# Optimization experiments

Hardware: AMD Instinct MI355X
Metric: run time of the kernel (lower is better)

The kernel has to match this reference:

```python
import jax, jax.numpy as jnp
import numpy as np


def setup_inputs() -> dict:
    key = jax.random.key(0)
    k1, k2, k3, k4 = jax.random.split(key, 4)
    bs, seq_len, num_heads, head_dim, num_pages = 16, 4096, 16, 128, 32768
    q = jax.random.normal(k1, (bs, num_heads, 1, head_dim), dtype=jnp.float32)
    kv_cache = jax.random.normal(k2, (2, num_pages, num_heads, head_dim), dtype=jnp.float32)
    k_indices = jax.random.randint(k3, (bs, seq_len), 0, num_pages, dtype=jnp.int64)
    v_indices = jax.random.randint(k4, (bs, seq_len), 0, num_pages, dtype=jnp.int64)
    return {"q": q, "kv_cache": kv_cache, "k_indices": k_indices, "v_indices": v_indices}


def reference(q, kv_cache, k_indices, v_indices):
    # Gather per-token K/V rows from the paged cache.
    k_cache = kv_cache[0]                      # [P, H, D]
    v_cache = kv_cache[1]                      # [P, H, D]
    k = k_cache[k_indices]                     # [B, S, H, D]
    v = v_cache[v_indices]                     # [B, S, H, D]
    head_dim = q.shape[-1]
    scale = 1.0 / jnp.sqrt(jnp.asarray(head_dim, dtype=q.dtype))
    # scores: [B, H, Q, S] (Q == 1 for decode); SDPA default: no mask, non-causal.
    scores = jnp.einsum("bhqd,bshd->bhqs", q, k) * scale
    probs = jax.nn.softmax(scores, axis=-1)
    out = jnp.einsum("bhqs,bshd->bhqd", probs, v)  # [B, H, Q, D]
    return out
```

## Files before the change

### kernel.cpp

```cpp
#include <hip/hip_runtime.h>
#include <math.h>

#define B 16
#define S 4096
#define H 16
#define D 128
#define P 32768

#define NSPLIT 8
#define WAVES_PER_BLOCK 4
#define TOK_PER_BLOCK (S / NSPLIT)
#define TOK_PER_WAVE (TOK_PER_BLOCK / WAVES_PER_BLOCK)

__global__ __launch_bounds__(256) void pa_partial(
    const float* __restrict__ q,
    const float* __restrict__ kv,
    const int* __restrict__ kidx,
    const int* __restrict__ vidx,
    float* __restrict__ ws)
{
    const int split = blockIdx.x;
    const int h     = blockIdx.y;
    const int b     = blockIdx.z;
    const int wave  = threadIdx.x >> 6;
    const int lane  = threadIdx.x & 63;

    const float scale = 0.08838834764831845f;

    const float* kbase = kv;
    const float* vbase = kv + (size_t)P * H * D;

    const float2 qv = *reinterpret_cast<const float2*>(
        q + ((size_t)b * H + h) * D + lane * 2);

    float  m   = -INFINITY;
    float  l   = 0.f;
    float2 acc = make_float2(0.f, 0.f);

    const int s0 = split * TOK_PER_BLOCK + wave * TOK_PER_WAVE;

    for (int half = 0; half < TOK_PER_WAVE / 64; ++half) {
        const int sbase = s0 + half * 64;
        const int myk = kidx[(size_t)b * S + sbase + lane];
        const int myv = vidx[(size_t)b * S + sbase + lane];

        #pragma unroll 4
        for (int t = 0; t < 64; ++t) {
            const int kp = __shfl(myk, t);
            const int vp = __shfl(myv, t);

            const float2 kvv = *reinterpret_cast<const float2*>(
                kbase + ((size_t)kp * H + h) * D + lane * 2);
            const float2 vvv = *reinterpret_cast<const float2*>(
                vbase + ((size_t)vp * H + h) * D + lane * 2);

            float partial = qv.x * kvv.x + qv.y * kvv.y;
            #pragma unroll
            for (int off = 32; off > 0; off >>= 1)
                partial += __shfl_xor(partial, off);

            const float score = partial * scale;
            const float mnew  = fmaxf(m, score);
            const float alpha = __expf(m - mnew);
            const float p     = __expf(score - mnew);
            l     = l * alpha + p;
            acc.x = acc.x * alpha + p * vvv.x;
            acc.y = acc.y * alpha + p * vvv.y;
            m     = mnew;
        }
    }

    __shared__ float lds_m[WAVES_PER_BLOCK];
    __shared__ float lds_l[WAVES_PER_BLOCK];
    __shared__ float lds_acc[WAVES_PER_BLOCK][D];

    lds_acc[wave][lane * 2]     = acc.x;
    lds_acc[wave][lane * 2 + 1] = acc.y;
    if (lane == 0) { lds_m[wave] = m; lds_l[wave] = l; }
    __syncthreads();

    float* out = ws + ((size_t)(b * H + h) * NSPLIT + split) * (D + 2);
    if (threadIdx.x < D) {
        const int d = threadIdx.x;
        const float M = fmaxf(fmaxf(lds_m[0], lds_m[1]),
                              fmaxf(lds_m[2], lds_m[3]));
        float L = 0.f, a = 0.f;
        #pragma unroll
        for (int w = 0; w < WAVES_PER_BLOCK; ++w) {
            const float e = __expf(lds_m[w] - M);
            L += lds_l[w] * e;
            a += lds_acc[w][d] * e;
        }
        out[d] = a;
        if (d == 0) { out[D] = M; out[D + 1] = L; }
    }
}

__global__ __launch_bounds__(128) void pa_reduce(
    const float* __restrict__ ws, float* __restrict__ out)
{
    const int bh = blockIdx.x;
    const int d  = threadIdx.x;
    const float* base = ws + (size_t)bh * NSPLIT * (D + 2);

    float M = -INFINITY;
    #pragma unroll
    for (int i = 0; i < NSPLIT; ++i)
        M = fmaxf(M, base[i * (D + 2) + D]);

    float L = 0.f, a = 0.f;
    #pragma unroll
    for (int i = 0; i < NSPLIT; ++i) {
        const float e = __expf(base[i * (D + 2) + D] - M);
        L += base[i * (D + 2) + D + 1] * e;
        a += base[i * (D + 2) + d] * e;
    }
    out[(size_t)bh * D + d] = a / L;
}

extern "C" void kernel_launch(void* const* d_in, const int* in_sizes, int n_in,
                              void* d_out, int out_size, void* d_ws, size_t ws_size,
                              hipStream_t stream) {
    const float* q    = (const float*)d_in[0];
    const float* kv   = (const float*)d_in[1];
    const int*   kidx = (const int*)d_in[2];
    const int*   vidx = (const int*)d_in[3];
    float*       out  = (float*)d_out;
    float*       ws   = (float*)d_ws;

    dim3 grid1(NSPLIT, H, B);
    pa_partial<<<grid1, 256, 0, stream>>>(q, kv, kidx, vidx, ws);
    pa_reduce<<<B * H, 128, 0, stream>>>(ws, out);
}
```

Baseline: 155.4 us.

## Counting-sort tokens by page to deduplicate KV reads and split K/V passes

Replaces the fused split-K flash-decode kernel with a seven-launch pipeline. It histograms, scans and scatters token indices into page-sorted lists, so each K page is read once as a full all-heads row and shared across batches and heads. V is gathered per batch in sorted page order. A K pass writes unnormalised exp(score) without subtracting a running max, a V pass accumulates weighted partial sums, and a final kernel normalises them. The intent is to cut scattered 512-byte gather traffic and reread K pages. The cost is many extra launches, atomics, an insertion-sort fixup and workspace traffic, and dropping max subtraction risks overflow for inputs with large scores.

```diff
diff --git a/kernel.cpp b/kernel.cpp
--- a/kernel.cpp
+++ b/kernel.cpp
@@ -1,121 +1,226 @@
 #include <hip/hip_runtime.h>
-#include <math.h>
 
 #define B 16
 #define S 4096
 #define H 16
 #define D 128
 #define P 32768
-
-#define NSPLIT 8
-#define WAVES_PER_BLOCK 4
-#define TOK_PER_BLOCK (S / NSPLIT)
-#define TOK_PER_WAVE (TOK_PER_BLOCK / WAVES_PER_BLOCK)
-
-__global__ __launch_bounds__(256) void pa_partial(
-    const float* __restrict__ q,
-    const float* __restrict__ kv,
-    const int* __restrict__ kidx,
-    const int* __restrict__ vidx,
-    float* __restrict__ ws)
-{
-    const int split = blockIdx.x;
-    const int h     = blockIdx.y;
-    const int b     = blockIdx.z;
-    const int wave  = threadIdx.x >> 6;
-    const int lane  = threadIdx.x & 63;
-
-    const float scale = 0.08838834764831845f;
-
-    const float* kbase = kv;
-    const float* vbase = kv + (size_t)P * H * D;
-
-    const float2 qv = *reinterpret_cast<const float2*>(
-        q + ((size_t)b * H + h) * D + lane * 2);
-
-    float  m   = -INFINITY;
-    float  l   = 0.f;
-    float2 acc = make_float2(0.f, 0.f);
-
-    const int s0 = split * TOK_PER_BLOCK + wave * TOK_PER_WAVE;
-
-    for (int half = 0; half < TOK_PER_WAVE / 64; ++half) {
-        const int sbase = s0 + half * 64;
-        const int myk = kidx[(size_t)b * S + sbase + lane];
-        const int myv = vidx[(size_t)b * S + sbase + lane];
-
-        #pragma unroll 4
-        for (int t = 0; t < 64; ++t) {
-            const int kp = __shfl(myk, t);
-            const int vp = __shfl(myv, t);
-
-            const float2 kvv = *reinterpret_cast<const float2*>(
-                kbase + ((size_t)kp * H + h) * D + lane * 2);
-            const float2 vvv = *reinterpret_cast<const float2*>(
-                vbase + ((size_t)vp * H + h) * D + lane * 2);
-
-            float partial = qv.x * kvv.x + qv.y * kvv.y;
-            #pragma unroll
-            for (int off = 32; off > 0; off >>= 1)
-                partial += __shfl_xor(partial, off);
-
-            const float score = partial * scale;
-            const float mnew  = fmaxf(m, score);
-            const float alpha = __expf(m - mnew);
-            const float p     = __expf(score - mnew);
-            l     = l * alpha + p;
-            acc.x = acc.x * alpha + p * vvv.x;
-            acc.y = acc.y * alpha + p * vvv.y;
-            m     = mnew;
+#define HD (H * D)
+#define NTOK (B * S)
+#define NVB (B * P)
+
+#define O_HIST_K 0
+#define O_HIST_V (O_HIST_K + P)
+#define O_EXCL_K (O_HIST_V + NVB)
+#define O_EXCL_V (O_EXCL_K + P)
+#define O_CUR_K  (O_EXCL_V + NVB)
+#define O_CUR_V  (O_CUR_K + P)
+#define O_SRT_K  (O_CUR_V + NVB)
+#define O_SRT_V  (O_SRT_K + NTOK)
+#define O_E      (O_SRT_V + NTOK)
+#define O_PART   (O_E + NTOK * H)
+
+#define SCALE 0.08838834764831845f
+
+__global__ __launch_bounds__(256) void hist_kernel(
+    const int* __restrict__ kidx, const int* __restrict__ vidx, int* ws)
+{
+    const int g = blockIdx.x * 256 + threadIdx.x;
+    atomicAdd(ws + O_HIST_K + kidx[g], 1);
+    const int b = g >> 12;
+    atomicAdd(ws + O_HIST_V + b * P + vidx[g], 1);
+}
+
+__global__ __launch_bounds__(1024) void scan_kernel(int* ws)
+{
+    const int blk = blockIdx.x, t = threadIdx.x;
+    const int* A;
+    int *E, *C;
+    int addbase;
+    if (blk < 16) {
+        A = ws + O_HIST_V + blk * P;
+        E = ws + O_EXCL_V + blk * P;
+        C = ws + O_CUR_V + blk * P;
+        addbase = blk * S;
+    } else {
+        A = ws + O_HIST_K; E = ws + O_EXCL_K; C = ws + O_CUR_K; addbase = 0;
+    }
+    const int base = t * 32;
+    int s = 0;
+    for (int i = 0; i < 32; ++i) s += A[base + i];
+    __shared__ int sd[1024];
+    sd[t] = s;
+    __syncthreads();
+    for (int d = 1; d < 1024; d <<= 1) {
+        const int v = (t >= d) ? sd[t - d] : 0;
+        __syncthreads();
+        sd[t] += v;
+        __syncthreads();
+    }
+    int run = sd[t] - s + addbase;
+    for (int i = 0; i < 32; ++i) {
+        E[base + i] = run;
+        C[base + i] = run;
+        run += A[base + i];
+    }
+}
+
+__global__ __launch_bounds__(256) void scatter_kernel(
+    const int* __restrict__ kidx, const int* __restrict__ vidx, int* ws)
+{
+    const int g = blockIdx.x * 256 + threadIdx.x;
+    const unsigned bs = (unsigned)(g & 0xFFFF);
+    const int kp = kidx[g];
+    int pos = atomicAdd(ws + O_CUR_K + kp, 1);
+    ((unsigned*)(ws + O_SRT_K))[pos] = ((unsigned)kp << 16) | bs;
+    const int b = g >> 12;
+    const int vp = vidx[g];
+    pos = atomicAdd(ws + O_CUR_V + b * P + vp, 1);
+    ((unsigned*)(ws + O_SRT_V))[pos] = ((unsigned)vp << 16) | bs;
+}
+
+__global__ __launch_bounds__(256) void sortfix_kernel(int* ws)
+{
+    const int t = blockIdx.x * 256 + threadIdx.x;
+    const int c = ws[O_HIST_V + t];
+    if (c < 2) return;
+    unsigned* L = (unsigned*)(ws + O_SRT_V) + ws[O_EXCL_V + t];
+    for (int i = 1; i < c; ++i) {
+        const unsigned key = L[i];
+        int j = i - 1;
+        while (j >= 0 && L[j] > key) { L[j + 1] = L[j]; --j; }
+        L[j + 1] = key;
+    }
+}
+
+__global__ __launch_bounds__(256) void kpass_kernel(
+    const float* __restrict__ q, const float* __restrict__ kv, int* ws)
+{
+    const unsigned* srt = (const unsigned*)(ws + O_SRT_K);
+    const int* excl = ws + O_EXCL_K;
+    float* e_ws = (float*)(ws + O_E);
+    const int j = blockIdx.x;
+    const int beg = excl[j * 32];
+    const int end = (j == 1023) ? NTOK : excl[j * 32 + 32];
+    if (beg >= end) return;
+    const int tid = threadIdx.x, h = tid >> 4, dc = tid & 15;
+    const int foff = h * D + dc * 8;
+
+    int i = beg;
+    int page = (int)(srt[i] >> 16);
+    const float* sp = kv + (size_t)page * HD + foff;
+    float4 na = *(const float4*)sp, nb = *(const float4*)(sp + 4);
+
+    while (i < end) {
+        int j2 = i + 1;
+        while (j2 < end && (int)(srt[j2] >> 16) == page) ++j2;
+        const float4 ca = na, cb = nb;
+        if (j2 < end) {
+            page = (int)(srt[j2] >> 16);
+            const float* p2 = kv + (size_t)page * HD + foff;
+            na = *(const float4*)p2; nb = *(const float4*)(p2 + 4);
         }
-    }
-
-    __shared__ float lds_m[WAVES_PER_BLOCK];
-    __shared__ float lds_l[WAVES_PER_BLOCK];
-    __shared__ float lds_acc[WAVES_PER_BLOCK][D];
-
-    lds_acc[wave][lane * 2]     = acc.x;
-    lds_acc[wave][lane * 2 + 1] = acc.y;
-    if (lane == 0) { lds_m[wave] = m; lds_l[wave] = l; }
+        for (int t = i; t < j2; ++t) {
+            const unsigned bs = srt[t] & 0xFFFFu;
+            const float* qp = q + ((bs >> 12) << 11) + foff;
+            const float4 qa = *(const float4*)qp;
+            const float4 qb = *(const float4*)(qp + 4);
+            float dot = qa.x * ca.x + qa.y * ca.y + qa.z * ca.z + qa.w * ca.w +
+                        qb.x * cb.x + qb.y * cb.y + qb.z * cb.z + qb.w * cb.w;
+            dot += __shfl_xor(dot, 1);
+            dot += __shfl_xor(dot, 2);
+            dot += __shfl_xor(dot, 4);
+            dot += __shfl_xor(dot, 8);
+            if (dc == 0) e_ws[bs * 16 + h] = __expf(dot * SCALE);
+        }
+        i = j2;
+    }
+}
+
+__global__ __launch_bounds__(256) void vpass_kernel(
+    const float* __restrict__ kv, int* ws)
+{
+    const float* vbase = kv + (size_t)P * HD;
+    const unsigned* srt = (const unsigned*)(ws + O_SRT_V);
+    const int* excl = ws + O_EXCL_V;
+    const float* e_ws = (const float*)(ws + O_E);
+    float* partial = (float*)(ws + O_PART);
+
+    const int blk = blockIdx.x;
+    const int b = blk >> 6, j = blk & 63;
+    const int beg = excl[b * P + j * 512];
+    const int end = (j == 63) ? (b + 1) * S : excl[b * P + (j + 1) * 512];
+    const int tid = threadIdx.x, h = tid >> 4, dc = tid & 15;
+    const int foff = h * D + dc * 8;
+
+    float4 a0 = make_float4(0.f, 0.f, 0.f, 0.f);
+    float4 a1 = make_float4(0.f, 0.f, 0.f, 0.f);
+
+    if (beg < end) {
+        int i = beg;
+        unsigned ent = srt[i];
+        int page = (int)(ent >> 16);
+        const float* sp = vbase + (size_t)page * HD + foff;
+        float4 na = *(const float4*)sp, nb = *(const float4*)(sp + 4);
+        while (i < end) {
+            const float4 ca = na, cb = nb;
+            const unsigned cent = ent;
+            const int nxt = i + 1;
+            if (nxt < end) {
+                ent = srt[nxt];
+                const int np = (int)(ent >> 16);
+                if (np != page) {
+                    page = np;
+                    const float* p2 = vbase + (size_t)np * HD + foff;
+                    na = *(const float4*)p2; nb = *(const float4*)(p2 + 4);
+                } else { na = ca; nb = cb; }
+            }
+            const float ev = e_ws[(cent & 0xFFFFu) * 16 + h];
+            a0.x += ev * ca.x; a0.y += ev * ca.y;
+            a0.z += ev * ca.z; a0.w += ev * ca.w;
+            a1.x += ev * cb.x; a1.y += ev * cb.y;
+            a1.z += ev * cb.z; a1.w += ev * cb.w;
+            i = nxt;
+        }
+    }
+    float* pp = partial + (size_t)blk * 2048 + foff;
+    *(float4*)pp = a0;
+    *(float4*)(pp + 4) = a1;
+}
+
+__global__ __launch_bounds__(256) void reduce_kernel(
+    const int* __restrict__ ws, float* __restrict__ out)
+{
+    const int b = blockIdx.x, t = threadIdx.x;
+    const float* e_b = (const float*)(ws + O_E) + (size_t)b * (S * H);
+    __shared__ float sd[256];
+    __shared__ float Lh[16];
+    float s = 0.f;
+    for (int k = 0; k < 256; ++k) s += e_b[k * 256 + t];
+    sd[t] = s;
     __syncthreads();
-
-    float* out = ws + ((size_t)(b * H + h) * NSPLIT + split) * (D + 2);
-    if (threadIdx.x < D) {
-        const int d = threadIdx.x;
-        const float M = fmaxf(fmaxf(lds_m[0], lds_m[1]),
-                              fmaxf(lds_m[2], lds_m[3]));
-        float L = 0.f, a = 0.f;
-        #pragma unroll
-        for (int w = 0; w < WAVES_PER_BLOCK; ++w) {
-            const float e = __expf(lds_m[w] - M);
-            L += lds_l[w] * e;
-            a += lds_acc[w][d] * e;
-        }
-        out[d] = a;
-        if (d == 0) { out[D] = M; out[D + 1] = L; }
-    }
-}
-
-__global__ __launch_bounds__(128) void pa_reduce(
-    const float* __restrict__ ws, float* __restrict__ out)
-{
-    const int bh = blockIdx.x;
-    const int d  = threadIdx.x;
-    const float* base = ws + (size_t)bh * NSPLIT * (D + 2);
-
-    float M = -INFINITY;
-    #pragma unroll
-    for (int i = 0; i < NSPLIT; ++i)
-        M = fmaxf(M, base[i * (D + 2) + D]);
-
-    float L = 0.f, a = 0.f;
-    #pragma unroll
-    for (int i = 0; i < NSPLIT; ++i) {
-        const float e = __expf(base[i * (D + 2) + D] - M);
-        L += base[i * (D + 2) + D + 1] * e;
-        a += base[i * (D + 2) + d] * e;
-    }
-    out[(size_t)bh * D + d] = a / L;
+    if (t < 16) {
+        float L = 0.f;
+        for (int g = 0; g < 16; ++g) L += sd[g * 16 + t];
+        Lh[t] = L;
+    }
+    __syncthreads();
+
+    const int o = t * 8;
+    const float inv = 1.f / Lh[o >> 7];
+    const float* pb = (const float*)(ws + O_PART) + (size_t)b * 64 * 2048;
+    float4 s0 = make_float4(0.f, 0.f, 0.f, 0.f);
+    float4 s1 = make_float4(0.f, 0.f, 0.f, 0.f);
+    for (int jj = 0; jj < 64; ++jj) {
+        const float* pp = pb + jj * 2048 + o;
+        const float4 p0 = *(const float4*)pp;
+        const float4 p1 = *(const float4*)(pp + 4);
+        s0.x += p0.x; s0.y += p0.y; s0.z += p0.z; s0.w += p0.w;
+        s1.x += p1.x; s1.y += p1.y; s1.z += p1.z; s1.w += p1.w;
+    }
+    float* op = out + (size_t)b * 2048 + o;
+    op[0] = s0.x * inv; op[1] = s0.y * inv; op[2] = s0.z * inv; op[3] = s0.w * inv;
+    op[4] = s1.x * inv; op[5] = s1.y * inv; op[6] = s1.z * inv; op[7] = s1.w * inv;
 }
 
 extern "C" void kernel_launch(void* const* d_in, const int* in_sizes, int n_in,
@@ -126,9 +231,14 @@
     const int*   kidx = (const int*)d_in[2];
     const int*   vidx = (const int*)d_in[3];
     float*       out  = (float*)d_out;
-    float*       ws   = (float*)d_ws;
-
-    dim3 grid1(NSPLIT, H, B);
-    pa_partial<<<grid1, 256, 0, stream>>>(q, kv, kidx, vidx, ws);
-    pa_reduce<<<B * H, 128, 0, stream>>>(ws, out);
-}
+    int*         ws   = (int*)d_ws;
+
+    hipMemsetAsync(ws, 0, (size_t)(P + NVB) * 4, stream);
+    hist_kernel   <<<NTOK / 256, 256, 0, stream>>>(kidx, vidx, ws);
+    scan_kernel   <<<17, 1024, 0, stream>>>(ws);
+    scatter_kernel<<<NTOK / 256, 256, 0, stream>>>(kidx, vidx, ws);
+    sortfix_kernel<<<NVB / 256, 256, 0, stream>>>(ws);
+    kpass_kernel  <<<1024, 256, 0, stream>>>(q, kv, ws);
+    vpass_kernel  <<<1024, 256, 0, stream>>>(kv, ws);
+    reduce_kernel <<<16, 256, 0, stream>>>(ws, out);
+}
```

New measurement: 227.7 us. 46.5% more time.
